# Kernel tuning notes

Measured on AMD Instinct MI355X. Metric: run time of the kernel, lower is better.

## Reference

```python
import jax, jax.numpy as jnp
import numpy as np

NEG_SLOPE = 0.2

def gat_layer(x, W, al, ar, src, dst, n_dst):
    # x: [Ns, Fin]; W: [Fin, H*D]; al/ar: [H, D]; src/dst: [E]
    H, D = al.shape
    h = (x @ W).reshape(-1, H, D)          # [Ns, H, D]
    h_dst = h[:n_dst]                       # dst nodes are prefix of src nodes (DGL block)
    el = (h * al).sum(-1)                   # [Ns, H]
    er = (h_dst * ar).sum(-1)               # [Nd, H]
    e = jax.nn.leaky_relu(el[src] + er[dst], NEG_SLOPE)  # [E, H]
    m = jax.ops.segment_max(e, dst, num_segments=n_dst)  # stable edge-softmax
    a = jnp.exp(e - m[dst])
    s = jax.ops.segment_sum(a, dst, num_segments=n_dst)
    alpha = a / s[dst]                      # [E, H]
    msg = h[src] * alpha[:, :, None]        # [E, H, D]
    out = jax.ops.segment_sum(msg, dst, num_segments=n_dst)  # [Nd, H, D]
    return out.reshape(n_dst, H * D)


def setup_inputs() -> dict:
    key = jax.random.key(0)
    ks = jax.random.split(key, 16)
    N0, N1, N2, N3 = 200000, 100000, 50000, 25000
    E0, E1, E2 = 1000000, 500000, 250000
    Fin, Dh, H, C = 256, 64, 3, 40
    inp = {}
    inp['x'] = jax.random.normal(ks[0], (N0, Fin), jnp.float32)
    inp['src0'] = jax.random.randint(ks[1], (E0,), 0, N0, jnp.int32)
    inp['dst0'] = jnp.sort(jax.random.randint(ks[2], (E0,), 0, N1, jnp.int32))
    inp['src1'] = jax.random.randint(ks[3], (E1,), 0, N1, jnp.int32)
    inp['dst1'] = jnp.sort(jax.random.randint(ks[4], (E1,), 0, N2, jnp.int32))
    inp['src2'] = jax.random.randint(ks[5], (E2,), 0, N2, jnp.int32)
    inp['dst2'] = jnp.sort(jax.random.randint(ks[6], (E2,), 0, N3, jnp.int32))
    sc = lambda f: np.float32(1.0 / np.sqrt(f))
    inp['W0'] = jax.random.normal(ks[7], (Fin, H * Dh), jnp.float32) * sc(Fin)
    inp['al0'] = jax.random.normal(ks[8], (H, Dh), jnp.float32) * sc(Dh)
    inp['ar0'] = jax.random.normal(ks[9], (H, Dh), jnp.float32) * sc(Dh)
    inp['W1'] = jax.random.normal(ks[10], (H * Dh, H * Dh), jnp.float32) * sc(H * Dh)
    inp['al1'] = jax.random.normal(ks[11], (H, Dh), jnp.float32) * sc(Dh)
    inp['ar1'] = jax.random.normal(ks[12], (H, Dh), jnp.float32) * sc(Dh)
    inp['W2'] = jax.random.normal(ks[13], (H * Dh, C), jnp.float32) * sc(H * Dh)
    inp['al2'] = jax.random.normal(ks[14], (1, C), jnp.float32) * sc(C)
    inp['ar2'] = jax.random.normal(ks[15], (1, C), jnp.float32) * sc(C)
    return inp


def reference(x, src0, dst0, src1, dst1, src2, dst2,
              W0, al0, ar0, W1, al1, ar1, W2, al2, ar2):
    N1, N2, N3 = 100000, 50000, 25000
    h = gat_layer(x, W0, al0, ar0, src0, dst0, N1)
    h = jax.nn.relu(h)  # dropout is identity in eval/deterministic mode
    h = gat_layer(h, W1, al1, ar1, src1, dst1, N2)
    h = jax.nn.relu(h)
    out = gat_layer(h, W2, al2, ar2, src2, dst2, N3)  # [N3, n_classes]
    return out
```

## Files before the change

kernel.cpp:

```cpp
#include <hip/hip_runtime.h>
#include <math.h>

#define DEV_INLINE __device__ __forceinline__

typedef __attribute__((ext_vector_type(8))) short short8v;
typedef __attribute__((ext_vector_type(4))) short short4v;
typedef __attribute__((ext_vector_type(4))) float float4v;

DEV_INLINE float wave_max_f(float v) {
#pragma unroll
  for (int o = 32; o > 0; o >>= 1) v = fmaxf(v, __shfl_xor(v, o, 64));
  return v;
}
DEV_INLINE float wave_sum_f(float v) {
#pragma unroll
  for (int o = 32; o > 0; o >>= 1) v += __shfl_xor(v, o, 64);
  return v;
}

DEV_INLINE unsigned short f2bf_rtn(float f) {
  unsigned u = __float_as_uint(f);
  u += 0x7FFFu + ((u >> 16) & 1u);
  return (unsigned short)(u >> 16);
}
DEV_INLINE float bf2f(unsigned short s) { return __uint_as_float(((unsigned)s) << 16); }

__global__ void conv_w(const float* __restrict__ W, short* __restrict__ Wh,
                       short* __restrict__ Wl, int K, int N) {
  int idx = blockIdx.x * 256 + threadIdx.x;
  if (idx >= K * N) return;
  int n = idx / K, k = idx - n * K;
  float w = W[(size_t)k * N + n];
  unsigned short h = f2bf_rtn(w);
  Wh[idx] = (short)h;
  Wl[idx] = (short)f2bf_rtn(w - bf2f(h));
}

__global__ void csr_build(const int* __restrict__ dst, int* __restrict__ off,
                          int E, int n_dst) {
  int i = blockIdx.x * 256 + threadIdx.x;
  if (i >= E) return;
  int d = dst[i];
  int p = (i == 0) ? -1 : dst[i - 1];
  for (int q = p + 1; q <= d; ++q) off[q] = i;
  if (i == E - 1)
    for (int q = d + 1; q <= n_dst; ++q) off[q] = E;
}

__global__ __launch_bounds__(256) void gemm_mfma(
    const float* __restrict__ A, const short* __restrict__ Bth,
    const short* __restrict__ Btl, float* __restrict__ C,
    int M, int N, int K) {
  __shared__ short As_h[128][40];
  __shared__ short As_l[128][40];
  __shared__ short Bs_h[64][40];
  __shared__ short Bs_l[64][40];
  const int tid = threadIdx.x;
  const int w = tid >> 6, lane = tid & 63;
  const int quad = lane >> 4, l16 = lane & 15;
  const int m0 = blockIdx.x * 128, n0 = blockIdx.y * 64;

  float4v acc[2][4];
#pragma unroll
  for (int mt = 0; mt < 2; ++mt)
#pragma unroll
    for (int nt = 0; nt < 4; ++nt)
#pragma unroll
      for (int r = 0; r < 4; ++r) acc[mt][nt][r] = 0.f;

  const int ar = tid >> 3;
  const int ac4 = (tid & 7) * 4;
  const int bn = tid >> 2;
  const int bk8 = (tid & 3) * 8;

  for (int k0 = 0; k0 < K; k0 += 32) {
    float4 a_reg[4];
#pragma unroll
    for (int p = 0; p < 4; ++p) {
      int gr = m0 + ar + p * 32;
      a_reg[p] = (gr < M) ? *(const float4*)(A + (size_t)gr * K + k0 + ac4)
                          : make_float4(0.f, 0.f, 0.f, 0.f);
    }
    short8v b_h, b_l;
    {
      int gn = n0 + bn;
      if (gn < N) {
        b_h = *(const short8v*)(Bth + (size_t)gn * K + k0 + bk8);
        b_l = *(const short8v*)(Btl + (size_t)gn * K + k0 + bk8);
      } else {
#pragma unroll
        for (int j = 0; j < 8; ++j) { b_h[j] = 0; b_l[j] = 0; }
      }
    }
    __syncthreads();
#pragma unroll
    for (int p = 0; p < 4; ++p) {
      int r = ar + p * 32;
      float vs[4] = {a_reg[p].x, a_reg[p].y, a_reg[p].z, a_reg[p].w};
      short4v hv, lv;
#pragma unroll
      for (int j = 0; j < 4; ++j) {
        unsigned short h = f2bf_rtn(vs[j]);
        hv[j] = (short)h;
        lv[j] = (short)f2bf_rtn(vs[j] - bf2f(h));
      }
      *(short4v*)&As_h[r][ac4] = hv;
      *(short4v*)&As_l[r][ac4] = lv;
    }
    *(short8v*)&Bs_h[bn][bk8] = b_h;
    *(short8v*)&Bs_l[bn][bk8] = b_l;
    __syncthreads();
    short8v afh[2], afl[2], bfh[4], bfl[4];
#pragma unroll
    for (int mt = 0; mt < 2; ++mt) {
      int row = w * 32 + mt * 16 + l16;
      afh[mt] = *(const short8v*)&As_h[row][quad * 8];
      afl[mt] = *(const short8v*)&As_l[row][quad * 8];
    }
#pragma unroll
    for (int nt = 0; nt < 4; ++nt) {
      int col = nt * 16 + l16;
      bfh[nt] = *(const short8v*)&Bs_h[col][quad * 8];
      bfl[nt] = *(const short8v*)&Bs_l[col][quad * 8];
    }
#pragma unroll
    for (int mt = 0; mt < 2; ++mt)
#pragma unroll
      for (int nt = 0; nt < 4; ++nt) {
        acc[mt][nt] = __builtin_amdgcn_mfma_f32_16x16x32_bf16(afh[mt], bfh[nt], acc[mt][nt], 0, 0, 0);
        acc[mt][nt] = __builtin_amdgcn_mfma_f32_16x16x32_bf16(afh[mt], bfl[nt], acc[mt][nt], 0, 0, 0);
        acc[mt][nt] = __builtin_amdgcn_mfma_f32_16x16x32_bf16(afl[mt], bfh[nt], acc[mt][nt], 0, 0, 0);
      }
  }
#pragma unroll
  for (int mt = 0; mt < 2; ++mt)
#pragma unroll
    for (int r = 0; r < 4; ++r) {
      int gr = m0 + w * 32 + mt * 16 + quad * 4 + r;
      if (gr < M) {
#pragma unroll
        for (int nt = 0; nt < 4; ++nt) {
          int gc = n0 + nt * 16 + l16;
          if (gc < N) C[(size_t)gr * N + gc] = acc[mt][nt][r];
        }
      }
    }
}

template <int H, int D>
__global__ __launch_bounds__(256) void elr_kernel(
    const float* __restrict__ h, const float* __restrict__ al,
    const float* __restrict__ ar, float* __restrict__ el,
    float* __restrict__ er, int M, int n_dst) {
  constexpr int F = H * D;
  constexpr int LANES = F / 4;
  const int w = threadIdx.x >> 6, lane = threadIdx.x & 63;
  const int m = blockIdx.x * 4 + w;
  if (m >= M) return;
  const int f4 = lane * 4;
  float4 hv = make_float4(0.f, 0.f, 0.f, 0.f);
  float4 av = hv, rv = hv;
  if (lane < LANES) {
    hv = *(const float4*)(h + (size_t)m * F + f4);
    av = *(const float4*)(al + f4);
    rv = *(const float4*)(ar + f4);
  }
  float pl = hv.x * av.x + hv.y * av.y + hv.z * av.z + hv.w * av.w;
  float pr = hv.x * rv.x + hv.y * rv.y + hv.z * rv.z + hv.w * rv.w;
#pragma unroll
  for (int o = 8; o >= 1; o >>= 1) {
    pl += __shfl_xor(pl, o, 16);
    pr += __shfl_xor(pr, o, 16);
  }
  if ((lane & 15) == 0 && f4 < F) {
    int hh = f4 / D;
    el[m * H + hh] = pl;
    if (m < n_dst) er[m * H + hh] = pr;
  }
}

template <int H, int D, bool RELU>
__global__ __launch_bounds__(256) void agg_kernel(
    const float* __restrict__ hsrc, const float* __restrict__ el,
    const float* __restrict__ er, const int* __restrict__ src,
    const int* __restrict__ off, float* __restrict__ out, int n_dst) {
  constexpr int F = H * D;
  constexpr int QL = F / 4;
  const int w = threadIdx.x >> 6, lane = threadIdx.x & 63;
  const int d = blockIdx.x * 4 + w;
  if (d >= n_dst) return;
  const int lo = off[d], hi = off[d + 1];
  const int f4 = lane * 4;
  const bool factive = lane < QL;
  const int hh = f4 / D;

  if (hi <= lo) {
    if (factive) *(float4*)(out + (size_t)d * F + f4) = make_float4(0.f, 0.f, 0.f, 0.f);
    return;
  }

  float erv[H], m_run[H], s_run[H];
  float4 acc = make_float4(0.f, 0.f, 0.f, 0.f);
#pragma unroll
  for (int h = 0; h < H; ++h) {
    erv[h] = er[d * H + h];
    m_run[h] = -INFINITY;
    s_run[h] = 0.f;
  }

  for (int base = lo; base < hi; base += 64) {
    const int i = base + lane;
    const bool valid = i < hi;
    const int sid = valid ? src[i] : 0;
    float a[H], rsel = 1.f;
#pragma unroll
    for (int h = 0; h < H; ++h) {
      float e = -INFINITY;
      if (valid) {
        e = el[sid * H + h] + erv[h];
        e = e > 0.f ? e : 0.2f * e;
      }
      float nm = fmaxf(m_run[h], wave_max_f(e));
      float r = __expf(m_run[h] - nm);
      a[h] = valid ? __expf(e - nm) : 0.f;
      s_run[h] = s_run[h] * r + wave_sum_f(a[h]);
      m_run[h] = nm;
      if (h == hh) rsel = r;
    }
    acc.x *= rsel; acc.y *= rsel; acc.z *= rsel; acc.w *= rsel;

    const int cnt = min(64, hi - base);
    for (int ei = 0; ei < cnt; ++ei) {
      const int sj = __shfl(sid, ei, 64);
      float aj[H];
#pragma unroll
      for (int h = 0; h < H; ++h) aj[h] = __shfl(a[h], ei, 64);
      float as = aj[0];
#pragma unroll
      for (int h = 1; h < H; ++h)
        if (hh == h) as = aj[h];
      if (factive) {
        const float4 hv = *(const float4*)(hsrc + (size_t)sj * F + f4);
        acc.x = fmaf(as, hv.x, acc.x);
        acc.y = fmaf(as, hv.y, acc.y);
        acc.z = fmaf(as, hv.z, acc.z);
        acc.w = fmaf(as, hv.w, acc.w);
      }
    }
  }

  float s = s_run[0];
#pragma unroll
  for (int h = 1; h < H; ++h)
    if (hh == h) s = s_run[h];
  if (factive) {
    float4 o;
    o.x = acc.x / s; o.y = acc.y / s; o.z = acc.z / s; o.w = acc.w / s;
    if (RELU) {
      o.x = fmaxf(o.x, 0.f); o.y = fmaxf(o.y, 0.f);
      o.z = fmaxf(o.z, 0.f); o.w = fmaxf(o.w, 0.f);
    }
    *(float4*)(out + (size_t)d * F + f4) = o;
  }
}

extern "C" void kernel_launch(void* const* d_in, const int* in_sizes, int n_in,
                              void* d_out, int out_size, void* d_ws, size_t ws_size,
                              hipStream_t stream) {
  const float* x   = (const float*)d_in[0];
  const int* src0  = (const int*)d_in[1];
  const int* dst0  = (const int*)d_in[2];
  const int* src1  = (const int*)d_in[3];
  const int* dst1  = (const int*)d_in[4];
  const int* src2  = (const int*)d_in[5];
  const int* dst2  = (const int*)d_in[6];
  const float* W0  = (const float*)d_in[7];
  const float* al0 = (const float*)d_in[8];
  const float* ar0 = (const float*)d_in[9];
  const float* W1  = (const float*)d_in[10];
  const float* al1 = (const float*)d_in[11];
  const float* ar1 = (const float*)d_in[12];
  const float* W2  = (const float*)d_in[13];
  const float* al2 = (const float*)d_in[14];
  const float* ar2 = (const float*)d_in[15];

  const int N0 = 200000, N1 = 100000, N2 = 50000, N3 = 25000;
  const int E0 = in_sizes[1], E1 = in_sizes[3], E2 = in_sizes[5];
  const int Fin = 256, F = 192, C = 40;

  float* ws     = (float*)d_ws;
  float* h_buf  = ws;
  float* o_buf  = h_buf + (size_t)N0 * F;
  float* el_buf = o_buf + (size_t)N1 * F;
  float* er_buf = el_buf + (size_t)N0 * 3;
  short* w0h    = (short*)(er_buf + (size_t)N1 * 3);
  short* w0l    = w0h + 192 * 256;
  short* w1h    = w0l + 192 * 256;
  short* w1l    = w1h + 192 * 192;
  short* w2h    = w1l + 192 * 192;
  short* w2l    = w2h + 40 * 192;
  int*   off0   = (int*)(w2l + 40 * 192);
  int*   off1   = off0 + (N1 + 1);
  int*   off2   = off1 + (N2 + 1);

  dim3 blk(256);

  conv_w<<<dim3((256 * 192 + 255) / 256), blk, 0, stream>>>(W0, w0h, w0l, Fin, F);
  conv_w<<<dim3((192 * 192 + 255) / 256), blk, 0, stream>>>(W1, w1h, w1l, F, F);
  conv_w<<<dim3((192 * 40 + 255) / 256), blk, 0, stream>>>(W2, w2h, w2l, F, C);
  csr_build<<<dim3((E0 + 255) / 256), blk, 0, stream>>>(dst0, off0, E0, N1);
  csr_build<<<dim3((E1 + 255) / 256), blk, 0, stream>>>(dst1, off1, E1, N2);
  csr_build<<<dim3((E2 + 255) / 256), blk, 0, stream>>>(dst2, off2, E2, N3);

  gemm_mfma<<<dim3((N0 + 127) / 128, F / 64), blk, 0, stream>>>(x, w0h, w0l, h_buf, N0, F, Fin);
  elr_kernel<3, 64><<<dim3((N0 + 3) / 4), blk, 0, stream>>>(h_buf, al0, ar0, el_buf, er_buf, N0, N1);
  agg_kernel<3, 64, true><<<dim3((N1 + 3) / 4), blk, 0, stream>>>(
      h_buf, el_buf, er_buf, src0, off0, o_buf, N1);

  gemm_mfma<<<dim3((N1 + 127) / 128, F / 64), blk, 0, stream>>>(o_buf, w1h, w1l, h_buf, N1, F, F);
  elr_kernel<3, 64><<<dim3((N1 + 3) / 4), blk, 0, stream>>>(h_buf, al1, ar1, el_buf, er_buf, N1, N2);
  agg_kernel<3, 64, true><<<dim3((N2 + 3) / 4), blk, 0, stream>>>(
      h_buf, el_buf, er_buf, src1, off1, o_buf, N2);

  gemm_mfma<<<dim3((N2 + 127) / 128, 1), blk, 0, stream>>>(o_buf, w2h, w2l, h_buf, N2, C, F);
  elr_kernel<1, 40><<<dim3((N2 + 3) / 4), blk, 0, stream>>>(h_buf, al2, ar2, el_buf, er_buf, N2, N3);
  agg_kernel<1, 40, false><<<dim3((N3 + 3) / 4), blk, 0, stream>>>(
      h_buf, el_buf, er_buf, src2, off2, (float*)d_out, N3);
}
```

Baseline: 773.0 us.

## Fuse attention logits into GEMM epilogue and rewrite edge aggregation

The GEMM now covers the full feature width in one tile and computes el/er in its epilogue, which removes the separate elr kernels and a re-read of h. LDS tiles use an XOR swizzle instead of padding. The three weight conversions and the three CSR builds are each merged into a single launch. Aggregation gives each destination node a 16-lane group, stages edge weights in shared memory and prefetches the next source row. It also drops the running-max softmax and uses plain exp, which can overflow for large logits.

Result: faster. 643.6 us (-16.7%).

```diff
diff --git a/kernel.cpp b/kernel.cpp
--- a/kernel.cpp
+++ b/kernel.cpp
@@ -4,19 +4,7 @@
 #define DEV_INLINE __device__ __forceinline__
 
 typedef __attribute__((ext_vector_type(8))) short short8v;
-typedef __attribute__((ext_vector_type(4))) short short4v;
 typedef __attribute__((ext_vector_type(4))) float float4v;
-
-DEV_INLINE float wave_max_f(float v) {
-#pragma unroll
-  for (int o = 32; o > 0; o >>= 1) v = fmaxf(v, __shfl_xor(v, o, 64));
-  return v;
-}
-DEV_INLINE float wave_sum_f(float v) {
-#pragma unroll
-  for (int o = 32; o > 0; o >>= 1) v += __shfl_xor(v, o, 64);
-  return v;
-}
 
 DEV_INLINE unsigned short f2bf_rtn(float f) {
   unsigned u = __float_as_uint(f);
@@ -25,242 +13,294 @@
 }
 DEV_INLINE float bf2f(unsigned short s) { return __uint_as_float(((unsigned)s) << 16); }
 
-__global__ void conv_w(const float* __restrict__ W, short* __restrict__ Wh,
-                       short* __restrict__ Wl, int K, int N) {
+DEV_INLINE int soff(int row, int oct) { return row * 32 + ((oct ^ (row & 3)) << 3); }
+
+__global__ void conv_w_all(const float* __restrict__ W0, const float* __restrict__ W1,
+                           const float* __restrict__ W2, short* __restrict__ w0h,
+                           short* __restrict__ w0l, short* __restrict__ w1h,
+                           short* __restrict__ w1l, short* __restrict__ w2h,
+                           short* __restrict__ w2l) {
+  const int S0 = 256 * 192, S1 = 192 * 192, S2 = 192 * 40;
   int idx = blockIdx.x * 256 + threadIdx.x;
-  if (idx >= K * N) return;
+  const float* W; short *Wh, *Wl; int K;
+  if (idx < S0) { W = W0; Wh = w0h; Wl = w0l; K = 256; }
+  else if (idx < S0 + S1) { idx -= S0; W = W1; Wh = w1h; Wl = w1l; K = 192; }
+  else if (idx < S0 + S1 + S2) { idx -= S0 + S1; W = W2; Wh = w2h; Wl = w2l; K = 192; }
+  else return;
   int n = idx / K, k = idx - n * K;
+  int N = (W == W0 || W == W1) ? 192 : 40;
   float w = W[(size_t)k * N + n];
   unsigned short h = f2bf_rtn(w);
   Wh[idx] = (short)h;
   Wl[idx] = (short)f2bf_rtn(w - bf2f(h));
 }
 
-__global__ void csr_build(const int* __restrict__ dst, int* __restrict__ off,
-                          int E, int n_dst) {
+__global__ void csr_all(const int* __restrict__ d0, const int* __restrict__ d1,
+                        const int* __restrict__ d2, int* __restrict__ o0,
+                        int* __restrict__ o1, int* __restrict__ o2,
+                        int E0, int E1, int E2, int n1, int n2, int n3) {
   int i = blockIdx.x * 256 + threadIdx.x;
-  if (i >= E) return;
+  const int* dst; int* off; int E, nd;
+  if (i < E0) { dst = d0; off = o0; E = E0; nd = n1; }
+  else if (i < E0 + E1) { i -= E0; dst = d1; off = o1; E = E1; nd = n2; }
+  else if (i < E0 + E1 + E2) { i -= E0 + E1; dst = d2; off = o2; E = E2; nd = n3; }
+  else return;
   int d = dst[i];
   int p = (i == 0) ? -1 : dst[i - 1];
   for (int q = p + 1; q <= d; ++q) off[q] = i;
   if (i == E - 1)
-    for (int q = d + 1; q <= n_dst; ++q) off[q] = E;
-}
-
-__global__ __launch_bounds__(256) void gemm_mfma(
+    for (int q = d + 1; q <= nd; ++q) off[q] = E;
+}
+
+template <int NT, int H>
+__global__ __launch_bounds__(256) void gemm_fused(
     const float* __restrict__ A, const short* __restrict__ Bth,
-    const short* __restrict__ Btl, float* __restrict__ C,
-    int M, int N, int K) {
-  __shared__ short As_h[128][40];
-  __shared__ short As_l[128][40];
-  __shared__ short Bs_h[64][40];
-  __shared__ short Bs_l[64][40];
+    const short* __restrict__ Btl, const float* __restrict__ al,
+    const float* __restrict__ ar, float* __restrict__ C,
+    float* __restrict__ el, float* __restrict__ er,
+    int M, int N, int K, int n_dst) {
+  constexpr int BN = NT * 16;
+  constexpr int BREP = (BN + 63) / 64;
+  constexpr int TPH = NT / H;
+  __shared__ short As_h[128 * 32], As_l[128 * 32];
+  __shared__ short Bs_h[BN * 32], Bs_l[BN * 32];
   const int tid = threadIdx.x;
   const int w = tid >> 6, lane = tid & 63;
   const int quad = lane >> 4, l16 = lane & 15;
-  const int m0 = blockIdx.x * 128, n0 = blockIdx.y * 64;
-
-  float4v acc[2][4];
+  const int m0 = blockIdx.x * 128;
+
+  float4v acc[2][NT];
 #pragma unroll
   for (int mt = 0; mt < 2; ++mt)
 #pragma unroll
-    for (int nt = 0; nt < 4; ++nt)
+    for (int nt = 0; nt < NT; ++nt)
 #pragma unroll
       for (int r = 0; r < 4; ++r) acc[mt][nt][r] = 0.f;
 
-  const int ar = tid >> 3;
-  const int ac4 = (tid & 7) * 4;
-  const int bn = tid >> 2;
-  const int bk8 = (tid & 3) * 8;
+  const int sr = tid >> 2;
+  const int oct = tid & 3;
 
   for (int k0 = 0; k0 < K; k0 += 32) {
-    float4 a_reg[4];
-#pragma unroll
-    for (int p = 0; p < 4; ++p) {
-      int gr = m0 + ar + p * 32;
-      a_reg[p] = (gr < M) ? *(const float4*)(A + (size_t)gr * K + k0 + ac4)
-                          : make_float4(0.f, 0.f, 0.f, 0.f);
-    }
-    short8v b_h, b_l;
-    {
-      int gn = n0 + bn;
-      if (gn < N) {
-        b_h = *(const short8v*)(Bth + (size_t)gn * K + k0 + bk8);
-        b_l = *(const short8v*)(Btl + (size_t)gn * K + k0 + bk8);
+    float4 a0[2], a1[2];
+#pragma unroll
+    for (int p = 0; p < 2; ++p) {
+      int gr = m0 + sr + p * 64;
+      if (gr < M) {
+        const float* ap = A + (size_t)gr * K + k0 + oct * 8;
+        a0[p] = *(const float4*)ap;
+        a1[p] = *(const float4*)(ap + 4);
       } else {
-#pragma unroll
-        for (int j = 0; j < 8; ++j) { b_h[j] = 0; b_l[j] = 0; }
+        a0[p] = make_float4(0.f, 0.f, 0.f, 0.f);
+        a1[p] = a0[p];
+      }
+    }
+    short8v bh[BREP], bl[BREP];
+#pragma unroll
+    for (int q = 0; q < BREP; ++q) {
+      int n = sr + q * 64;
+      if (n < BN) {
+        if (n < N) {
+          bh[q] = *(const short8v*)(Bth + (size_t)n * K + k0 + oct * 8);
+          bl[q] = *(const short8v*)(Btl + (size_t)n * K + k0 + oct * 8);
+        } else {
+#pragma unroll
+          for (int j = 0; j < 8; ++j) { bh[q][j] = 0; bl[q][j] = 0; }
+        }
       }
     }
     __syncthreads();
 #pragma unroll
-    for (int p = 0; p < 4; ++p) {
-      int r = ar + p * 32;
-      float vs[4] = {a_reg[p].x, a_reg[p].y, a_reg[p].z, a_reg[p].w};
-      short4v hv, lv;
-#pragma unroll
-      for (int j = 0; j < 4; ++j) {
+    for (int p = 0; p < 2; ++p) {
+      int r = sr + p * 64;
+      float vs[8] = {a0[p].x, a0[p].y, a0[p].z, a0[p].w,
+                     a1[p].x, a1[p].y, a1[p].z, a1[p].w};
+      short8v hv, lv;
+#pragma unroll
+      for (int j = 0; j < 8; ++j) {
         unsigned short h = f2bf_rtn(vs[j]);
         hv[j] = (short)h;
         lv[j] = (short)f2bf_rtn(vs[j] - bf2f(h));
       }
-      *(short4v*)&As_h[r][ac4] = hv;
-      *(short4v*)&As_l[r][ac4] = lv;
-    }
-    *(short8v*)&Bs_h[bn][bk8] = b_h;
-    *(short8v*)&Bs_l[bn][bk8] = b_l;
+      *(short8v*)(As_h + soff(r, oct)) = hv;
+      *(short8v*)(As_l + soff(r, oct)) = lv;
+    }
+#pragma unroll
+    for (int q = 0; q < BREP; ++q) {
+      int n = sr + q * 64;
+      if (n < BN) {
+        *(short8v*)(Bs_h + soff(n, oct)) = bh[q];
+        *(short8v*)(Bs_l + soff(n, oct)) = bl[q];
+      }
+    }
     __syncthreads();
-    short8v afh[2], afl[2], bfh[4], bfl[4];
+    short8v afh[2], afl[2];
 #pragma unroll
     for (int mt = 0; mt < 2; ++mt) {
       int row = w * 32 + mt * 16 + l16;
-      afh[mt] = *(const short8v*)&As_h[row][quad * 8];
-      afl[mt] = *(const short8v*)&As_l[row][quad * 8];
-    }
-#pragma unroll
-    for (int nt = 0; nt < 4; ++nt) {
+      afh[mt] = *(const short8v*)(As_h + soff(row, quad));
+      afl[mt] = *(const short8v*)(As_l + soff(row, quad));
+    }
+#pragma unroll
+    for (int nt = 0; nt < NT; ++nt) {
       int col = nt * 16 + l16;
-      bfh[nt] = *(const short8v*)&Bs_h[col][quad * 8];
-      bfl[nt] = *(const short8v*)&Bs_l[col][quad * 8];
-    }
-#pragma unroll
-    for (int mt = 0; mt < 2; ++mt)
-#pragma unroll
-      for (int nt = 0; nt < 4; ++nt) {
-        acc[mt][nt] = __builtin_amdgcn_mfma_f32_16x16x32_bf16(afh[mt], bfh[nt], acc[mt][nt], 0, 0, 0);
-        acc[mt][nt] = __builtin_amdgcn_mfma_f32_16x16x32_bf16(afh[mt], bfl[nt], acc[mt][nt], 0, 0, 0);
-        acc[mt][nt] = __builtin_amdgcn_mfma_f32_16x16x32_bf16(afl[mt], bfh[nt], acc[mt][nt], 0, 0, 0);
-      }
+      short8v bfh = *(const short8v*)(Bs_h + soff(col, quad));
+      short8v bfl = *(const short8v*)(Bs_l + soff(col, quad));
+#pragma unroll
+      for (int mt = 0; mt < 2; ++mt) {
+        acc[mt][nt] = __builtin_amdgcn_mfma_f32_16x16x32_bf16(afh[mt], bfh, acc[mt][nt], 0, 0, 0);
+        acc[mt][nt] = __builtin_amdgcn_mfma_f32_16x16x32_bf16(afh[mt], bfl, acc[mt][nt], 0, 0, 0);
+        acc[mt][nt] = __builtin_amdgcn_mfma_f32_16x16x32_bf16(afl[mt], bfh, acc[mt][nt], 0, 0, 0);
+      }
+    }
+  }
+
+  float av[NT], rv[NT];
+#pragma unroll
+  for (int nt = 0; nt < NT; ++nt) {
+    int col = nt * 16 + l16;
+    av[nt] = (col < N) ? al[col] : 0.f;
+    rv[nt] = (col < N) ? ar[col] : 0.f;
   }
 #pragma unroll
   for (int mt = 0; mt < 2; ++mt)
 #pragma unroll
     for (int r = 0; r < 4; ++r) {
-      int gr = m0 + w * 32 + mt * 16 + quad * 4 + r;
-      if (gr < M) {
-#pragma unroll
-        for (int nt = 0; nt < 4; ++nt) {
-          int gc = n0 + nt * 16 + l16;
-          if (gc < N) C[(size_t)gr * N + gc] = acc[mt][nt][r];
+      int gm = m0 + w * 32 + mt * 16 + quad * 4 + r;
+      if (gm >= M) continue;
+      float pl[H], pr[H];
+#pragma unroll
+      for (int h = 0; h < H; ++h) { pl[h] = 0.f; pr[h] = 0.f; }
+#pragma unroll
+      for (int nt = 0; nt < NT; ++nt) {
+        int h = nt / TPH;
+        pl[h] = fmaf(acc[mt][nt][r], av[nt], pl[h]);
+        pr[h] = fmaf(acc[mt][nt][r], rv[nt], pr[h]);
+      }
+#pragma unroll
+      for (int h = 0; h < H; ++h) {
+#pragma unroll
+        for (int o = 8; o >= 1; o >>= 1) {
+          pl[h] += __shfl_xor(pl[h], o, 16);
+          pr[h] += __shfl_xor(pr[h], o, 16);
         }
       }
-    }
-}
-
-template <int H, int D>
-__global__ __launch_bounds__(256) void elr_kernel(
-    const float* __restrict__ h, const float* __restrict__ al,
-    const float* __restrict__ ar, float* __restrict__ el,
-    float* __restrict__ er, int M, int n_dst) {
-  constexpr int F = H * D;
-  constexpr int LANES = F / 4;
-  const int w = threadIdx.x >> 6, lane = threadIdx.x & 63;
-  const int m = blockIdx.x * 4 + w;
-  if (m >= M) return;
-  const int f4 = lane * 4;
-  float4 hv = make_float4(0.f, 0.f, 0.f, 0.f);
-  float4 av = hv, rv = hv;
-  if (lane < LANES) {
-    hv = *(const float4*)(h + (size_t)m * F + f4);
-    av = *(const float4*)(al + f4);
-    rv = *(const float4*)(ar + f4);
-  }
-  float pl = hv.x * av.x + hv.y * av.y + hv.z * av.z + hv.w * av.w;
-  float pr = hv.x * rv.x + hv.y * rv.y + hv.z * rv.z + hv.w * rv.w;
-#pragma unroll
-  for (int o = 8; o >= 1; o >>= 1) {
-    pl += __shfl_xor(pl, o, 16);
-    pr += __shfl_xor(pr, o, 16);
-  }
-  if ((lane & 15) == 0 && f4 < F) {
-    int hh = f4 / D;
-    el[m * H + hh] = pl;
-    if (m < n_dst) er[m * H + hh] = pr;
-  }
+      if (l16 == 0) {
+#pragma unroll
+        for (int h = 0; h < H; ++h) {
+          el[gm * H + h] = pl[h];
+          if (gm < n_dst) er[gm * H + h] = pr[h];
+        }
+      }
+#pragma unroll
+      for (int nt = 0; nt < NT; ++nt) {
+        int col = nt * 16 + l16;
+        if (col < N) C[(size_t)gm * N + col] = acc[mt][nt][r];
+      }
+    }
 }
 
 template <int H, int D, bool RELU>
-__global__ __launch_bounds__(256) void agg_kernel(
+__global__ __launch_bounds__(256) void agg2_kernel(
     const float* __restrict__ hsrc, const float* __restrict__ el,
     const float* __restrict__ er, const int* __restrict__ src,
     const int* __restrict__ off, float* __restrict__ out, int n_dst) {
   constexpr int F = H * D;
-  constexpr int QL = F / 4;
-  const int w = threadIdx.x >> 6, lane = threadIdx.x & 63;
-  const int d = blockIdx.x * 4 + w;
+  constexpr int NP = (F + 63) / 64;
+  __shared__ float wbuf[16][16][H];
+  __shared__ int sbuf[16][16];
+  const int g = threadIdx.x >> 4, l = threadIdx.x & 15;
+  const int d = blockIdx.x * 16 + g;
   if (d >= n_dst) return;
   const int lo = off[d], hi = off[d + 1];
-  const int f4 = lane * 4;
-  const bool factive = lane < QL;
-  const int hh = f4 / D;
 
   if (hi <= lo) {
-    if (factive) *(float4*)(out + (size_t)d * F + f4) = make_float4(0.f, 0.f, 0.f, 0.f);
+#pragma unroll
+    for (int p = 0; p < NP; ++p) {
+      int c4 = (p * 16 + l) * 4;
+      if (c4 < F) *(float4*)(out + (size_t)d * F + c4) = make_float4(0.f, 0.f, 0.f, 0.f);
+    }
     return;
   }
 
-  float erv[H], m_run[H], s_run[H];
-  float4 acc = make_float4(0.f, 0.f, 0.f, 0.f);
+  float erv[H], s_part[H];
 #pragma unroll
   for (int h = 0; h < H; ++h) {
     erv[h] = er[d * H + h];
-    m_run[h] = -INFINITY;
-    s_run[h] = 0.f;
-  }
-
-  for (int base = lo; base < hi; base += 64) {
-    const int i = base + lane;
+    s_part[h] = 0.f;
+  }
+  float4 acc[NP];
+#pragma unroll
+  for (int p = 0; p < NP; ++p) acc[p] = make_float4(0.f, 0.f, 0.f, 0.f);
+
+  for (int base = lo; base < hi; base += 16) {
+    const int i = base + l;
     const bool valid = i < hi;
     const int sid = valid ? src[i] : 0;
-    float a[H], rsel = 1.f;
 #pragma unroll
     for (int h = 0; h < H; ++h) {
-      float e = -INFINITY;
+      float e = 0.f;
       if (valid) {
         e = el[sid * H + h] + erv[h];
         e = e > 0.f ? e : 0.2f * e;
-      }
-      float nm = fmaxf(m_run[h], wave_max_f(e));
-      float r = __expf(m_run[h] - nm);
-      a[h] = valid ? __expf(e - nm) : 0.f;
-      s_run[h] = s_run[h] * r + wave_sum_f(a[h]);
-      m_run[h] = nm;
-      if (h == hh) rsel = r;
-    }
-    acc.x *= rsel; acc.y *= rsel; acc.z *= rsel; acc.w *= rsel;
-
-    const int cnt = min(64, hi - base);
+        e = __expf(e);
+      }
+      s_part[h] += e;
+      wbuf[g][l][h] = e;
+    }
+    sbuf[g][l] = sid;
+
+    const int cnt = min(16, hi - base);
+    int sj = sbuf[g][0];
+    float4 hv[NP], hn[NP];
+#pragma unroll
+    for (int p = 0; p < NP; ++p) {
+      int c4 = (p * 16 + l) * 4;
+      hv[p] = (c4 < F) ? *(const float4*)(hsrc + (size_t)sj * F + c4)
+                       : make_float4(0.f, 0.f, 0.f, 0.f);
+    }
     for (int ei = 0; ei < cnt; ++ei) {
-      const int sj = __shfl(sid, ei, 64);
-      float aj[H];
-#pragma unroll
-      for (int h = 0; h < H; ++h) aj[h] = __shfl(a[h], ei, 64);
-      float as = aj[0];
-#pragma unroll
-      for (int h = 1; h < H; ++h)
-        if (hh == h) as = aj[h];
-      if (factive) {
-        const float4 hv = *(const float4*)(hsrc + (size_t)sj * F + f4);
-        acc.x = fmaf(as, hv.x, acc.x);
-        acc.y = fmaf(as, hv.y, acc.y);
-        acc.z = fmaf(as, hv.z, acc.z);
-        acc.w = fmaf(as, hv.w, acc.w);
-      }
-    }
-  }
-
-  float s = s_run[0];
-#pragma unroll
-  for (int h = 1; h < H; ++h)
-    if (hh == h) s = s_run[h];
-  if (factive) {
-    float4 o;
-    o.x = acc.x / s; o.y = acc.y / s; o.z = acc.z / s; o.w = acc.w / s;
-    if (RELU) {
-      o.x = fmaxf(o.x, 0.f); o.y = fmaxf(o.y, 0.f);
-      o.z = fmaxf(o.z, 0.f); o.w = fmaxf(o.w, 0.f);
-    }
-    *(float4*)(out + (size_t)d * F + f4) = o;
+      if (ei + 1 < cnt) {
+        int sj2 = sbuf[g][ei + 1];
+#pragma unroll
+        for (int p = 0; p < NP; ++p) {
+          int c4 = (p * 16 + l) * 4;
+          hn[p] = (c4 < F) ? *(const float4*)(hsrc + (size_t)sj2 * F + c4)
+                           : make_float4(0.f, 0.f, 0.f, 0.f);
+        }
+      }
+#pragma unroll
+      for (int p = 0; p < NP; ++p) {
+        int c4 = (p * 16 + l) * 4;
+        float wc = wbuf[g][ei][c4 / D];
+        acc[p].x = fmaf(wc, hv[p].x, acc[p].x);
+        acc[p].y = fmaf(wc, hv[p].y, acc[p].y);
+        acc[p].z = fmaf(wc, hv[p].z, acc[p].z);
+        acc[p].w = fmaf(wc, hv[p].w, acc[p].w);
+      }
+#pragma unroll
+      for (int p = 0; p < NP; ++p) hv[p] = hn[p];
+    }
+  }
+
+#pragma unroll
+  for (int h = 0; h < H; ++h)
+#pragma unroll
+    for (int o = 8; o >= 1; o >>= 1) s_part[h] += __shfl_xor(s_part[h], o, 16);
+
+#pragma unroll
+  for (int p = 0; p < NP; ++p) {
+    int c4 = (p * 16 + l) * 4;
+    if (c4 < F) {
+      float inv = 1.f / s_part[c4 / D];
+      float4 o;
+      o.x = acc[p].x * inv; o.y = acc[p].y * inv;
+      o.z = acc[p].z * inv; o.w = acc[p].w * inv;
+      if (RELU) {
+        o.x = fmaxf(o.x, 0.f); o.y = fmaxf(o.y, 0.f);
+        o.z = fmaxf(o.z, 0.f); o.w = fmaxf(o.w, 0.f);
+      }
+      *(float4*)(out + (size_t)d * F + c4) = o;
+    }
   }
 }
 
@@ -305,25 +345,24 @@
 
   dim3 blk(256);
 
-  conv_w<<<dim3((256 * 192 + 255) / 256), blk, 0, stream>>>(W0, w0h, w0l, Fin, F);
-  conv_w<<<dim3((192 * 192 + 255) / 256), blk, 0, stream>>>(W1, w1h, w1l, F, F);
-  conv_w<<<dim3((192 * 40 + 255) / 256), blk, 0, stream>>>(W2, w2h, w2l, F, C);
-  csr_build<<<dim3((E0 + 255) / 256), blk, 0, stream>>>(dst0, off0, E0, N1);
-  csr_build<<<dim3((E1 + 255) / 256), blk, 0, stream>>>(dst1, off1, E1, N2);
-  csr_build<<<dim3((E2 + 255) / 256), blk, 0, stream>>>(dst2, off2, E2, N3);
-
-  gemm_mfma<<<dim3((N0 + 127) / 128, F / 64), blk, 0, stream>>>(x, w0h, w0l, h_buf, N0, F, Fin);
-  elr_kernel<3, 64><<<dim3((N0 + 3) / 4), blk, 0, stream>>>(h_buf, al0, ar0, el_buf, er_buf, N0, N1);
-  agg_kernel<3, 64, true><<<dim3((N1 + 3) / 4), blk, 0, stream>>>(
+  const int WTOT = 256 * 192 + 192 * 192 + 192 * 40;
+  conv_w_all<<<dim3((WTOT + 255) / 256), blk, 0, stream>>>(W0, W1, W2, w0h, w0l, w1h, w1l, w2h, w2l);
+  const int ETOT = E0 + E1 + E2;
+  csr_all<<<dim3((ETOT + 255) / 256), blk, 0, stream>>>(dst0, dst1, dst2, off0, off1, off2,
+                                                        E0, E1, E2, N1, N2, N3);
+
+  gemm_fused<12, 3><<<dim3((N0 + 127) / 128), blk, 0, stream>>>(
+      x, w0h, w0l, al0, ar0, h_buf, el_buf, er_buf, N0, F, Fin, N1);
+  agg2_kernel<3, 64, true><<<dim3((N1 + 15) / 16), blk, 0, stream>>>(
       h_buf, el_buf, er_buf, src0, off0, o_buf, N1);
 
-  gemm_mfma<<<dim3((N1 + 127) / 128, F / 64), blk, 0, stream>>>(o_buf, w1h, w1l, h_buf, N1, F, F);
-  elr_kernel<3, 64><<<dim3((N1 + 3) / 4), blk, 0, stream>>>(h_buf, al1, ar1, el_buf, er_buf, N1, N2);
-  agg_kernel<3, 64, true><<<dim3((N2 + 3) / 4), blk, 0, stream>>>(
+  gemm_fused<12, 3><<<dim3((N1 + 127) / 128), blk, 0, stream>>>(
+      o_buf, w1h, w1l, al1, ar1, h_buf, el_buf, er_buf, N1, F, F, N2);
+  agg2_kernel<3, 64, true><<<dim3((N2 + 15) / 16), blk, 0, stream>>>(
       h_buf, el_buf, er_buf, src1, off1, o_buf, N2);
 
-  gemm_mfma<<<dim3((N2 + 127) / 128, 1), blk, 0, stream>>>(o_buf, w2h, w2l, h_buf, N2, C, F);
-  elr_kernel<1, 40><<<dim3((N2 + 3) / 4), blk, 0, stream>>>(h_buf, al2, ar2, el_buf, er_buf, N2, N3);
-  agg_kernel<1, 40, false><<<dim3((N3 + 3) / 4), blk, 0, stream>>>(
+  gemm_fused<3, 1><<<dim3((N2 + 127) / 128), blk, 0, stream>>>(
+      o_buf, w2h, w2l, al2, ar2, h_buf, el_buf, er_buf, N2, C, F, N3);
+  agg2_kernel<1, 40, false><<<dim3((N3 + 15) / 16), blk, 0, stream>>>(
       h_buf, el_buf, er_buf, src2, off2, (float*)d_out, N3);
 }
```
